# Performance work log

Hardware: AMD Instinct MI355X
Metric: run time of the kernel (lower is better)

The kernel has to match this reference:

```python
import jax, jax.numpy as jnp
import numpy as np

B, S, D = 2, 2048, 2048
H, DK, DV, L = 16, 128, 128, 64


def setup_inputs() -> dict:
    key = jax.random.key(0)
    ks = jax.random.split(key, 12)
    s = lambda k, shape, fan_in: jax.random.normal(k, shape, jnp.float32) / np.sqrt(fan_in)
    return {
        "queries": jax.random.normal(ks[0], (B, S, D), jnp.float32),
        "keys": jax.random.normal(ks[1], (B, S, D), jnp.float32),
        "values": jax.random.normal(ks[2], (B, S, D), jnp.float32),
        "Wq": s(ks[3], (D, H * DK), D), "bq": jnp.zeros((H * DK,), jnp.float32),
        "Wlk": s(ks[4], (D, H * L), D), "blk": jnp.zeros((H * L,), jnp.float32),
        "Wlv": s(ks[5], (D, H * L), D), "blv": jnp.zeros((H * L,), jnp.float32),
        "Wkr": s(ks[6], (L, DK), L),
        "Wvr": s(ks[7], (L, DV), L),
        "Wout": s(ks[8], (H * DV, D), H * DV), "bout": jnp.zeros((D,), jnp.float32),
    }


def reference(queries, keys, values, Wq, bq, Wlk, blk, Wlv, blv, Wkr, Wvr, Wout, bout):
    b, sq, _ = queries.shape
    sk = keys.shape[1]
    # projections -> [b, h, s, d]
    q = (queries @ Wq + bq).reshape(b, sq, H, DK).transpose(0, 2, 1, 3)
    lk = (keys @ Wlk + blk).reshape(b, sk, H, L).transpose(0, 2, 1, 3)
    lv = (values @ Wlv + blv).reshape(b, sk, H, L).transpose(0, 2, 1, 3)
    k = lk @ Wkr  # [b,h,sk,DK] latent -> key reconstruction
    v = lv @ Wvr  # [b,h,sk,DV]
    scores = jnp.einsum('bhqd,bhkd->bhqk', q, k) / np.sqrt(DK).astype(np.float32)
    causal = jnp.triu(jnp.ones((sq, sk), dtype=bool), k=1)
    scores = jnp.where(causal, -jnp.inf, scores)
    attn = jax.nn.softmax(scores, axis=-1)
    out = jnp.einsum('bhqk,bhkd->bhqd', attn, v)
    out = out.transpose(0, 2, 1, 3).reshape(b, sq, H * DV)
    return out @ Wout + bout
```

## Files before the change

### kernel.cpp

```cpp
#include <hip/hip_runtime.h>
#include <cstdint>
#include <cstddef>

typedef _Float16 f16;
typedef __attribute__((ext_vector_type(8))) _Float16 f16x8;
typedef __attribute__((ext_vector_type(4))) _Float16 f16x4;
typedef __attribute__((ext_vector_type(4))) float f32x4;

constexpr int kB  = 2;
constexpr int kS  = 2048;
constexpr int kD  = 2048;
constexpr int kH  = 16;
constexpr int kL  = 64;
constexpr int kHL = kH * kL;
constexpr int kBS = kB * kS;

__device__ __forceinline__ void load_lds16(const void* g, void* l) {
  __builtin_amdgcn_global_load_lds((const __attribute__((address_space(1))) void*)g,
                                   (__attribute__((address_space(3))) void*)l, 16, 0, 0);
}

__device__ __forceinline__ f32x4 mfma16(f16x8 a, f16x8 b, f32x4 c) {
  return __builtin_amdgcn_mfma_f32_16x16x32_f16(a, b, c, 0, 0, 0);
}

__global__ void cast4(const float* __restrict__ a, const float* __restrict__ b,
                      const float* __restrict__ c, const float* __restrict__ d,
                      f16* __restrict__ oa, f16* __restrict__ ob,
                      f16* __restrict__ oc, f16* __restrict__ od) {
  const int z = blockIdx.z;
  int i = blockIdx.x * 256 + threadIdx.x;
  if (z == 3 && i >= kD * kD / 4) return;
  const float* in = z == 0 ? a : z == 1 ? b : z == 2 ? c : d;
  f16* out = z == 0 ? oa : z == 1 ? ob : z == 2 ? oc : od;
  float4 f = ((const float4*)in)[i];
  f16x4 o; o[0] = (f16)f.x; o[1] = (f16)f.y; o[2] = (f16)f.z; o[3] = (f16)f.w;
  ((f16x4*)out)[i] = o;
}

__device__ __forceinline__ void transpose_body(const float* __restrict__ in,
                                               f16* __restrict__ out, int R, int C) {
  const int r0 = blockIdx.y * 64, c0 = blockIdx.x * 64;
  __shared__ float tile[64][65];
  const int t = threadIdx.x;
  const int cc = t & 63, rr = t >> 6;
#pragma unroll
  for (int p = 0; p < 16; p++) {
    int r = p * 4 + rr;
    tile[r][cc] = in[(size_t)(r0 + r) * C + c0 + cc];
  }
  __syncthreads();
#pragma unroll
  for (int p = 0; p < 16; p++) {
    int c = p * 4 + rr;
    out[(size_t)(c0 + c) * R + r0 + cc] = (f16)tile[cc][c];
  }
}

__global__ __launch_bounds__(256) void transpose3(const float* __restrict__ Wlk,
                                                  const float* __restrict__ Wlv,
                                                  const float* __restrict__ Wout,
                                                  f16* __restrict__ Wlkt,
                                                  f16* __restrict__ Wlvt,
                                                  f16* __restrict__ WoutT) {
  const int z = blockIdx.z;
  if (z < 2 && blockIdx.x >= 16) return;
  if (z == 0) transpose_body(Wlk, Wlkt, 2048, 1024);
  else if (z == 1) transpose_body(Wlv, Wlvt, 2048, 1024);
  else transpose_body(Wout, WoutT, 2048, 2048);
}

__global__ void fold_bq(const float* __restrict__ bq, const float* __restrict__ Wkr,
                        float* __restrict__ bql) {
  int hl = blockIdx.x * 256 + threadIdx.x;
  if (hl >= kHL) return;
  int h = hl >> 6, l = hl & 63;
  float s = 0.f;
  for (int c = 0; c < 128; c++) s += bq[h * 128 + c] * Wkr[l * 128 + c];
  bql[hl] = s;
}

__global__ __launch_bounds__(256) void fold2(const float* __restrict__ Wkr,
                                             const float* __restrict__ Wvr,
                                             const f16* __restrict__ Wq16,
                                             const f16* __restrict__ WoutT,
                                             f16* __restrict__ Wqlt,
                                             f16* __restrict__ W2t) {
  __shared__ f16 sA[64 * 136];
  __shared__ f16 sB[128 * 128];
  const int z = blockIdx.z;
  const int h = blockIdx.y;
  const int d0 = blockIdx.x * 128;
  const float* Wsm = z ? Wvr : Wkr;
  const f16* Bsrc = (z ? WoutT : Wq16) + h * 128;
  const int tid = threadIdx.x;
  const int w = tid >> 6, lane = tid & 63;
  const int quad = lane >> 4, l16 = lane & 15;

#pragma unroll
  for (int it = 0; it < 8; it++) {
    int i = it * 256 + tid;
    float4 f = ((const float4*)Wsm)[i];
    int e = i * 4, r = e >> 7, c = e & 127;
    f16x4 o; o[0] = (f16)f.x; o[1] = (f16)f.y; o[2] = (f16)f.z; o[3] = (f16)f.w;
    *(f16x4*)&sA[r * 136 + c] = o;
  }
#pragma unroll
  for (int c = 0; c < 8; c++) {
    int rbase = w * 32 + c * 4;
    load_lds16(Bsrc + (size_t)(d0 + rbase + (lane >> 4)) * 2048 + (lane & 15) * 8,
               &sB[rbase * 128]);
  }
  __syncthreads();

  if (z == 0) {
    f32x4 acc[4][2];
    for (int mt = 0; mt < 4; mt++)
      for (int nt = 0; nt < 2; nt++) acc[mt][nt] = (f32x4){0.f, 0.f, 0.f, 0.f};
#pragma unroll
    for (int ks = 0; ks < 4; ks++) {
      f16x8 af[4], bf[2];
#pragma unroll
      for (int mt = 0; mt < 4; mt++)
        af[mt] = *(const f16x8*)&sA[(mt * 16 + l16) * 136 + ks * 32 + quad * 8];
#pragma unroll
      for (int nt = 0; nt < 2; nt++)
        bf[nt] = *(const f16x8*)&sB[(w * 32 + nt * 16 + l16) * 128 + ks * 32 + quad * 8];
#pragma unroll
      for (int mt = 0; mt < 4; mt++)
#pragma unroll
        for (int nt = 0; nt < 2; nt++) acc[mt][nt] = mfma16(af[mt], bf[nt], acc[mt][nt]);
    }
#pragma unroll
    for (int mt = 0; mt < 4; mt++)
#pragma unroll
      for (int nt = 0; nt < 2; nt++)
#pragma unroll
        for (int r = 0; r < 4; r++) {
          int row = mt * 16 + quad * 4 + r;
          int col = d0 + w * 32 + nt * 16 + l16;
          Wqlt[(size_t)(h * 64 + row) * 2048 + col] = (f16)acc[mt][nt][r];
        }
  } else {
    f32x4 acc[2][4];
    for (int mt = 0; mt < 2; mt++)
      for (int nt = 0; nt < 4; nt++) acc[mt][nt] = (f32x4){0.f, 0.f, 0.f, 0.f};
#pragma unroll
    for (int ks = 0; ks < 4; ks++) {
      f16x8 af[2], bf[4];
#pragma unroll
      for (int mt = 0; mt < 2; mt++)
        af[mt] = *(const f16x8*)&sB[(w * 32 + mt * 16 + l16) * 128 + ks * 32 + quad * 8];
#pragma unroll
      for (int nt = 0; nt < 4; nt++)
        bf[nt] = *(const f16x8*)&sA[(nt * 16 + l16) * 136 + ks * 32 + quad * 8];
#pragma unroll
      for (int mt = 0; mt < 2; mt++)
#pragma unroll
        for (int nt = 0; nt < 4; nt++) acc[mt][nt] = mfma16(af[mt], bf[nt], acc[mt][nt]);
    }
#pragma unroll
    for (int mt = 0; mt < 2; mt++)
#pragma unroll
      for (int nt = 0; nt < 4; nt++)
#pragma unroll
        for (int r = 0; r < 4; r++) {
          int row = d0 + w * 32 + mt * 16 + quad * 4 + r;
          int col = nt * 16 + l16;
          W2t[(size_t)row * 1024 + h * 64 + col] = (f16)acc[mt][nt][r];
        }
  }
}

template <typename OutT, bool HAS_BIAS>
__device__ __forceinline__ void gemm8p_body(const f16* __restrict__ A, const f16* __restrict__ Bt,
                                            const float* __restrict__ bias, OutT* __restrict__ C,
                                            int N, int K, int m0, int n0) {
  __shared__ f16 sA[3 * 256 * 64];
  __shared__ f16 sB[3 * 128 * 64];
  const int tid = threadIdx.x;
  const int w = tid >> 6, lane = tid & 63;
  const int quad = lane >> 4, l16 = lane & 15;
  const int wm = w >> 2, wn = w & 3;
  const int sw0 = ((quad ^ (l16 & 7)) << 3);
  const int sw1 = (((4 + quad) ^ (l16 & 7)) << 3);

  const int srow = lane >> 3;
  const int schunk = (lane & 7) ^ srow;
  const f16* aG = A + (size_t)(m0 + w * 8 + srow) * K + schunk * 8;
  const f16* bG = Bt + (size_t)(n0 + w * 8 + srow) * K + schunk * 8;
  const int ldsOff = (w * 8) * 64 + lane * 8;

  f32x4 acc[8][2];
#pragma unroll
  for (int i = 0; i < 8; i++) {
    acc[i][0] = (f32x4){0.f, 0.f, 0.f, 0.f};
    acc[i][1] = (f32x4){0.f, 0.f, 0.f, 0.f};
  }

#define STAGE_A(b, k0, j) load_lds16(aG + (size_t)((j) * 64) * K + (k0), \
                                     &sA[(b) * 16384 + (j) * 4096 + ldsOff])
#define STAGE_B(b, k0, j) load_lds16(bG + (size_t)((j) * 64) * K + (k0), \
                                     &sB[(b) * 8192 + (j) * 4096 + ldsOff])
#define PHASE_PRE()  do { __builtin_amdgcn_sched_barrier(0); __builtin_amdgcn_s_barrier(); \
    asm volatile("s_waitcnt lgkmcnt(0)" ::: "memory"); __builtin_amdgcn_sched_barrier(0); \
    __builtin_amdgcn_s_setprio(1); } while (0)
#define PHASE_POST() do { __builtin_amdgcn_s_setprio(0); __builtin_amdgcn_sched_barrier(0); \
    __builtin_amdgcn_s_barrier(); } while (0)

  const int nt = K >> 6;
#pragma unroll
  for (int j = 0; j < 4; j++) STAGE_A(0, 0, j);
  STAGE_B(0, 0, 0); STAGE_B(0, 0, 1);
#pragma unroll
  for (int j = 0; j < 4; j++) STAGE_A(1, 64, j);
  STAGE_B(1, 64, 0); STAGE_B(1, 64, 1);
  asm volatile("s_waitcnt vmcnt(6)" ::: "memory");
  __builtin_amdgcn_sched_barrier(0);
  __builtin_amdgcn_s_barrier();
  __builtin_amdgcn_sched_barrier(0);

  int bc = 0, bs = 2;
  for (int t = 0; t < nt; ++t) {
    const f16* a = &sA[bc * 16384];
    const f16* b = &sB[bc * 8192];
    const bool st = (t + 2) < nt;
    const int kS = (t + 2) << 6;
    f16x8 af[8], bf;

#pragma unroll
    for (int mt = 0; mt < 8; mt++)
      af[mt] = *(const f16x8*)&a[(wm * 128 + mt * 16 + l16) * 64 + sw0];
    bf = *(const f16x8*)&b[(wn * 32 + l16) * 64 + sw0];
    if (st) { STAGE_A(bs, kS, 0); STAGE_A(bs, kS, 1); }
    PHASE_PRE();
#pragma unroll
    for (int mt = 0; mt < 8; mt++) acc[mt][0] = mfma16(af[mt], bf, acc[mt][0]);
    PHASE_POST();

    bf = *(const f16x8*)&b[(wn * 32 + 16 + l16) * 64 + sw0];
    if (st) { STAGE_A(bs, kS, 2); STAGE_A(bs, kS, 3); }
    PHASE_PRE();
#pragma unroll
    for (int mt = 0; mt < 8; mt++) acc[mt][1] = mfma16(af[mt], bf, acc[mt][1]);
    PHASE_POST();

#pragma unroll
    for (int mt = 0; mt < 8; mt++)
      af[mt] = *(const f16x8*)&a[(wm * 128 + mt * 16 + l16) * 64 + sw1];
    bf = *(const f16x8*)&b[(wn * 32 + l16) * 64 + sw1];
    if (st) STAGE_B(bs, kS, 0);
    PHASE_PRE();
#pragma unroll
    for (int mt = 0; mt < 8; mt++) acc[mt][0] = mfma16(af[mt], bf, acc[mt][0]);
    PHASE_POST();

    bf = *(const f16x8*)&b[(wn * 32 + 16 + l16) * 64 + sw1];
    if (st) STAGE_B(bs, kS, 1);
    PHASE_PRE();
#pragma unroll
    for (int mt = 0; mt < 8; mt++) acc[mt][1] = mfma16(af[mt], bf, acc[mt][1]);
    __builtin_amdgcn_s_setprio(0);
    if (t + 1 < nt) {
      if (st) asm volatile("s_waitcnt vmcnt(6)" ::: "memory");
      else    asm volatile("s_waitcnt vmcnt(0)" ::: "memory");
    }
    __builtin_amdgcn_sched_barrier(0);
    __builtin_amdgcn_s_barrier();
    __builtin_amdgcn_sched_barrier(0);

    bc = bc == 2 ? 0 : bc + 1;
    bs = bs == 2 ? 0 : bs + 1;
  }
#undef STAGE_A
#undef STAGE_B
#undef PHASE_PRE
#undef PHASE_POST

#pragma unroll
  for (int mt = 0; mt < 8; mt++) {
#pragma unroll
    for (int nh = 0; nh < 2; nh++) {
      int col = n0 + wn * 32 + nh * 16 + l16;
      float bv = HAS_BIAS ? bias[col] : 0.f;
#pragma unroll
      for (int r = 0; r < 4; r++) {
        int row = m0 + wm * 128 + mt * 16 + quad * 4 + r;
        C[(size_t)row * N + col] = (OutT)(acc[mt][nh][r] + bv);
      }
    }
  }
}

__device__ __forceinline__ int xcd_swizzle(int flat, int nwg) {
  const int cpx = nwg >> 3;
  return (flat & 7) * cpx + (flat >> 3);
}

__global__ __launch_bounds__(512) void gemm3_f16(
    const f16* __restrict__ A0, const f16* __restrict__ A1, const f16* __restrict__ A2,
    const f16* __restrict__ B0, const f16* __restrict__ B1, const f16* __restrict__ B2,
    const float* __restrict__ c0, const float* __restrict__ c1, const float* __restrict__ c2,
    f16* __restrict__ C0, f16* __restrict__ C1, f16* __restrict__ C2, int N, int K) {
  const f16* A = blockIdx.z == 0 ? A0 : blockIdx.z == 1 ? A1 : A2;
  const f16* Bt = blockIdx.z == 0 ? B0 : blockIdx.z == 1 ? B1 : B2;
  const float* bias = blockIdx.z == 0 ? c0 : blockIdx.z == 1 ? c1 : c2;
  f16* C = blockIdx.z == 0 ? C0 : blockIdx.z == 1 ? C1 : C2;
  const int nx = gridDim.x;
  int swz = xcd_swizzle(blockIdx.y * nx + blockIdx.x, nx * gridDim.y);
  gemm8p_body<f16, true>(A, Bt, bias, C, N, K, (swz / nx) * 256, (swz % nx) * 128);
}

__global__ __launch_bounds__(512) void gemm_f32(const f16* __restrict__ A,
                                                const f16* __restrict__ Bt,
                                                const float* __restrict__ bias,
                                                float* __restrict__ C, int N, int K) {
  const int nx = gridDim.x;
  int swz = xcd_swizzle(blockIdx.y * nx + blockIdx.x, nx * gridDim.y);
  gemm8p_body<float, true>(A, Bt, bias, C, N, K, (swz / nx) * 256, (swz % nx) * 128);
}

__global__ __launch_bounds__(256) void transpose_lv(const f16* __restrict__ LV,
                                                    f16* __restrict__ LVt) {
  const int bh = blockIdx.y, b = bh >> 4, h = bh & 15;
  const int s0 = blockIdx.x * 64;
  __shared__ f16 tile[64][65];
  const int t = threadIdx.x;
  const int c0 = t & 63, r0 = t >> 6;
#pragma unroll
  for (int r = 0; r < 16; r++) {
    int s = r * 4 + r0;
    tile[s][c0] = LV[(size_t)(b * kS + s0 + s) * kHL + h * kL + c0];
  }
  __syncthreads();
#pragma unroll
  for (int r = 0; r < 16; r++) {
    int vl = r * 4 + r0;
    LVt[((size_t)bh * kL + vl) * kS + s0 + c0] = tile[c0][vl];
  }
}

__global__ __launch_bounds__(256) void attn(const f16* __restrict__ Qlat,
                                            const f16* __restrict__ LK,
                                            const f16* __restrict__ LVt,
                                            f16* __restrict__ Ctx) {
  const int bh = blockIdx.y, b = bh >> 4, h = bh & 15;
  const int pair = blockIdx.x;
  const int tid = threadIdx.x;
  const int w = tid >> 6, lane = tid & 63;
  const int quad = lane >> 4, l16 = lane & 15;

  __shared__ f16 sK[2][64 * 64];
  __shared__ f16 sV[2][64 * 64];
  __shared__ f16 sP[4][16 * 72];

  const f16* qbase = Qlat + (size_t)b * kS * kHL + h * kL;
  const f16* kbase = LK + (size_t)b * kS * kHL + h * kL;
  const f16* vbase = LVt + (size_t)bh * kL * kS;

  const float cscale = 0.08838834764831845f * 1.4426950408889634f;
  const int rowA = lane >> 3;
  const int colSw = (((lane & 7) ^ (lane >> 3)) << 3);
  const int sw0 = ((quad ^ (l16 & 7)) << 3);
  const int sw1 = (((4 + quad) ^ (l16 & 7)) << 3);

  for (int which = 0; which < 2; which++) {
    const int t = which ? (31 - pair) : pair;
    const int q0 = t * 64;
    const int qrow = q0 + w * 16 + l16;
    const int qg = qrow;
    const int ntile = t + 1;

    f16x8 aq[2];
#pragma unroll
    for (int ks = 0; ks < 2; ks++)
      aq[ks] = *(const f16x8*)(qbase + (size_t)qrow * kHL + ks * 32 + quad * 8);

    f32x4 acc[4];
    for (int nt = 0; nt < 4; nt++) acc[nt] = (f32x4){0.f, 0.f, 0.f, 0.f};
    float m_s = -3.0e38f;
    float l_part = 0.f;

    __syncthreads();
    {
      const int rl = w * 16;
      load_lds16(kbase + (size_t)(rl + rowA) * kHL + colSw, &sK[0][rl * 64]);
      load_lds16(vbase + (size_t)(rl + rowA) * kS + colSw, &sV[0][rl * 64]);
      load_lds16(kbase + (size_t)(rl + 8 + rowA) * kHL + colSw, &sK[0][(rl + 8) * 64]);
      load_lds16(vbase + (size_t)(rl + 8 + rowA) * kS + colSw, &sV[0][(rl + 8) * 64]);
    }
    int cur = 0;

    for (int it = 0; it < ntile; ++it) {
      const int kv0 = it * 64;
      __syncthreads();

      if (it + 1 < ntile) {
        const int nkv = kv0 + 64;
        f16* dK = &sK[cur ^ 1][0];
        f16* dV = &sV[cur ^ 1][0];
        const int rl = w * 16;
        load_lds16(kbase + (size_t)(nkv + rl + rowA) * kHL + colSw, dK + rl * 64);
        load_lds16(vbase + (size_t)(rl + rowA) * kS + nkv + colSw, dV + rl * 64);
        load_lds16(kbase + (size_t)(nkv + rl + 8 + rowA) * kHL + colSw, dK + (rl + 8) * 64);
        load_lds16(vbase + (size_t)(rl + 8 + rowA) * kS + nkv + colSw, dV + (rl + 8) * 64);
      }
      const f16* sKc = &sK[cur][0];
      const f16* sVc = &sV[cur][0];

      f32x4 sc[4];
      for (int nt = 0; nt < 4; nt++) sc[nt] = (f32x4){0.f, 0.f, 0.f, 0.f};
#pragma unroll
      for (int ks = 0; ks < 2; ks++) {
        const int sw = ks ? sw1 : sw0;
        f16x8 bk[4];
#pragma unroll
        for (int nt = 0; nt < 4; nt++)
          bk[nt] = *(const f16x8*)&sKc[(nt * 16 + l16) * 64 + sw];
        __builtin_amdgcn_s_setprio(1);
#pragma unroll
        for (int nt = 0; nt < 4; nt++) sc[nt] = mfma16(bk[nt], aq[ks], sc[nt]);
        __builtin_amdgcn_s_setprio(0);
      }

      if (kv0 == q0) {
#pragma unroll
        for (int nt = 0; nt < 4; nt++) {
#pragma unroll
          for (int r = 0; r < 4; r++) {
            int kvg = kv0 + nt * 16 + quad * 4 + r;
            if (kvg > qg) sc[nt][r] = -1.0e30f;
          }
        }
      }

      float tm = -3.0e38f;
#pragma unroll
      for (int nt = 0; nt < 4; nt++)
        tm = fmaxf(tm, fmaxf(fmaxf(sc[nt][0], sc[nt][1]), fmaxf(sc[nt][2], sc[nt][3])));
      tm = fmaxf(tm, __shfl_xor(tm, 16));
      tm = fmaxf(tm, __shfl_xor(tm, 32));
      const float tms = tm * cscale;

      if (!__all(tms <= m_s)) {
        const float mnew = fmaxf(m_s, tms);
        const float alpha = __builtin_amdgcn_exp2f(m_s - mnew);
        m_s = mnew;
        l_part *= alpha;
        float ar[4];
#pragma unroll
        for (int r = 0; r < 4; r++) ar[r] = __shfl(alpha, quad * 4 + r);
#pragma unroll
        for (int nt = 0; nt < 4; nt++)
#pragma unroll
          for (int r = 0; r < 4; r++) acc[nt][r] *= ar[r];
      }

      float ps = 0.f;
#pragma unroll
      for (int nt = 0; nt < 4; nt++) {
        f16x4 pk;
#pragma unroll
        for (int r = 0; r < 4; r++) {
          float p = __builtin_amdgcn_exp2f(__builtin_fmaf(sc[nt][r], cscale, -m_s));
          ps += p;
          pk[r] = (f16)p;
        }
        *(f16x4*)&sP[w][l16 * 72 + nt * 16 + quad * 4] = pk;
      }
      l_part += ps;

#pragma unroll
      for (int ks = 0; ks < 2; ks++) {
        const int sw = ks ? sw1 : sw0;
        f16x8 ap = *(const f16x8*)&sP[w][l16 * 72 + ks * 32 + quad * 8];
        f16x8 bv[4];
#pragma unroll
        for (int nt = 0; nt < 4; nt++)
          bv[nt] = *(const f16x8*)&sVc[(nt * 16 + l16) * 64 + sw];
        __builtin_amdgcn_s_setprio(1);
#pragma unroll
        for (int nt = 0; nt < 4; nt++) acc[nt] = mfma16(ap, bv[nt], acc[nt]);
        __builtin_amdgcn_s_setprio(0);
      }
      cur ^= 1;
    }

    float lfull = l_part;
    lfull += __shfl_xor(lfull, 16);
    lfull += __shfl_xor(lfull, 32);
    float inv[4];
#pragma unroll
    for (int r = 0; r < 4; r++) inv[r] = 1.f / __shfl(lfull, quad * 4 + r);
#pragma unroll
    for (int r = 0; r < 4; r++) {
      int qout = q0 + w * 16 + quad * 4 + r;
      size_t base = (size_t)(b * kS + qout) * kHL + h * kL;
#pragma unroll
      for (int nt = 0; nt < 4; nt++)
        Ctx[base + nt * 16 + l16] = (f16)(acc[nt][r] * inv[r]);
    }
  }
}

extern "C" void kernel_launch(void* const* d_in, const int* in_sizes, int n_in,
                              void* d_out, int out_size, void* d_ws, size_t ws_size,
                              hipStream_t stream) {
  (void)in_sizes; (void)n_in; (void)out_size; (void)ws_size;
  const float* queries = (const float*)d_in[0];
  const float* keys    = (const float*)d_in[1];
  const float* values  = (const float*)d_in[2];
  const float* Wq      = (const float*)d_in[3];
  const float* bq      = (const float*)d_in[4];
  const float* Wlk     = (const float*)d_in[5];
  const float* blk     = (const float*)d_in[6];
  const float* Wlv     = (const float*)d_in[7];
  const float* blv     = (const float*)d_in[8];
  const float* Wkr     = (const float*)d_in[9];
  const float* Wvr     = (const float*)d_in[10];
  const float* Wout    = (const float*)d_in[11];
  const float* bout    = (const float*)d_in[12];

  char* ws = (char*)d_ws;
  size_t off = 0;
  auto alloc = [&](size_t bytes) {
    void* p = ws + off;
    off += (bytes + 255) & ~(size_t)255;
    return p;
  };
  f16* qb    = (f16*)alloc((size_t)kBS * kD * 2);
  f16* kb    = (f16*)alloc((size_t)kBS * kD * 2);
  f16* vb    = (f16*)alloc((size_t)kBS * kD * 2);
  f16* Wqlt  = (f16*)alloc((size_t)kHL * kD * 2);
  f16* Wlkt  = (f16*)alloc((size_t)kHL * kD * 2);
  f16* Wlvt  = (f16*)alloc((size_t)kHL * kD * 2);
  f16* W2t   = (f16*)alloc((size_t)kD * kHL * 2);
  float* bql = (float*)alloc(kHL * 4);
  f16* Qlat  = (f16*)alloc((size_t)kBS * kHL * 2);
  f16* LKb   = (f16*)alloc((size_t)kBS * kHL * 2);
  f16* LVb   = (f16*)alloc((size_t)kBS * kHL * 2);
  f16* Wq16  = Qlat;
  f16* WoutT = LKb;
  f16* LVtb = qb;
  f16* Ctx  = kb;

  const int n4 = kBS * kD / 4;
  cast4<<<dim3(n4 / 256, 1, 4), 256, 0, stream>>>(queries, keys, values, Wq, qb, kb, vb, Wq16);
  transpose3<<<dim3(32, 32, 3), 256, 0, stream>>>(Wlk, Wlv, Wout, Wlkt, Wlvt, WoutT);
  fold_bq<<<kHL / 256, 256, 0, stream>>>(bq, Wkr, bql);
  fold2<<<dim3(16, 16, 2), 256, 0, stream>>>(Wkr, Wvr, Wq16, WoutT, Wqlt, W2t);

  gemm3_f16<<<dim3(kHL / 128, kBS / 256, 3), 512, 0, stream>>>(
      qb, kb, vb, Wqlt, Wlkt, Wlvt, bql, blk, blv, Qlat, LKb, LVb, kHL, kD);

  transpose_lv<<<dim3(kS / 64, kB * kH), 256, 0, stream>>>(LVb, LVtb);
  attn<<<dim3(16, kB * kH), 256, 0, stream>>>(Qlat, LKb, LVtb, Ctx);
  gemm_f32<<<dim3(kD / 128, kBS / 256), 512, 0, stream>>>(Ctx, W2t, bout, (float*)d_out, kD, kHL);
}
```

Measured before the change: 395.6 us.

## Switch GEMM warp layout to 4x2 with 64x64 per-wave tiles and two phases

Changes the 8-wave arrangement in the 256x128 block GEMM from 2x4 (128x32 per wave) to 4x2 (64x64 per wave), so each wave loads 4 A and 4 B fragments and runs 16 MFMAs per k-half. Each k-step now has two barrier-separated phases instead of four, with global-to-LDS staging regrouped to match. The aim is fewer LDS fragment reads per MFMA and fewer barriers per k-step. In exchange each phase holds more fragment registers live and the epilogue write pattern changes.

After: 364.3 us. 7.9% less time.

```diff
diff --git a/kernel.cpp b/kernel.cpp
--- a/kernel.cpp
+++ b/kernel.cpp
@@ -181,7 +181,7 @@
   const int tid = threadIdx.x;
   const int w = tid >> 6, lane = tid & 63;
   const int quad = lane >> 4, l16 = lane & 15;
-  const int wm = w >> 2, wn = w & 3;
+  const int wm = w >> 1, wn = w & 1;
   const int sw0 = ((quad ^ (l16 & 7)) << 3);
   const int sw1 = (((4 + quad) ^ (l16 & 7)) << 3);
 
@@ -191,30 +191,30 @@
   const f16* bG = Bt + (size_t)(n0 + w * 8 + srow) * K + schunk * 8;
   const int ldsOff = (w * 8) * 64 + lane * 8;
 
-  f32x4 acc[8][2];
-#pragma unroll
-  for (int i = 0; i < 8; i++) {
-    acc[i][0] = (f32x4){0.f, 0.f, 0.f, 0.f};
-    acc[i][1] = (f32x4){0.f, 0.f, 0.f, 0.f};
-  }
-
-#define STAGE_A(b, k0, j) load_lds16(aG + (size_t)((j) * 64) * K + (k0), \
-                                     &sA[(b) * 16384 + (j) * 4096 + ldsOff])
-#define STAGE_B(b, k0, j) load_lds16(bG + (size_t)((j) * 64) * K + (k0), \
-                                     &sB[(b) * 8192 + (j) * 4096 + ldsOff])
-#define PHASE_PRE()  do { __builtin_amdgcn_sched_barrier(0); __builtin_amdgcn_s_barrier(); \
-    asm volatile("s_waitcnt lgkmcnt(0)" ::: "memory"); __builtin_amdgcn_sched_barrier(0); \
-    __builtin_amdgcn_s_setprio(1); } while (0)
-#define PHASE_POST() do { __builtin_amdgcn_s_setprio(0); __builtin_amdgcn_sched_barrier(0); \
-    __builtin_amdgcn_s_barrier(); } while (0)
+  f32x4 acc[4][4];
+#pragma unroll
+  for (int i = 0; i < 4; i++)
+#pragma unroll
+    for (int j = 0; j < 4; j++) acc[i][j] = (f32x4){0.f, 0.f, 0.f, 0.f};
+
+#define STAGE_A4(b, k0) do {                                                   \
+    load_lds16(aG + (k0),                  &sA[(b) * 16384 + ldsOff]);          \
+    load_lds16(aG + (size_t)64 * K + (k0), &sA[(b) * 16384 + 4096 + ldsOff]);   \
+    load_lds16(aG + (size_t)128 * K + (k0), &sA[(b) * 16384 + 8192 + ldsOff]);  \
+    load_lds16(aG + (size_t)192 * K + (k0), &sA[(b) * 16384 + 12288 + ldsOff]); \
+  } while (0)
+#define STAGE_B2(b, k0) do {                                                   \
+    load_lds16(bG + (k0),                  &sB[(b) * 8192 + ldsOff]);           \
+    load_lds16(bG + (size_t)64 * K + (k0), &sB[(b) * 8192 + 4096 + ldsOff]);    \
+  } while (0)
+#define PHASE_SYNC() do { __builtin_amdgcn_sched_barrier(0);                   \
+    __builtin_amdgcn_s_barrier();                                              \
+    asm volatile("s_waitcnt lgkmcnt(0)" ::: "memory");                         \
+    __builtin_amdgcn_sched_barrier(0); } while (0)
 
   const int nt = K >> 6;
-#pragma unroll
-  for (int j = 0; j < 4; j++) STAGE_A(0, 0, j);
-  STAGE_B(0, 0, 0); STAGE_B(0, 0, 1);
-#pragma unroll
-  for (int j = 0; j < 4; j++) STAGE_A(1, 64, j);
-  STAGE_B(1, 64, 0); STAGE_B(1, 64, 1);
+  STAGE_A4(0, 0); STAGE_B2(0, 0);
+  STAGE_A4(1, 64); STAGE_B2(1, 64);
   asm volatile("s_waitcnt vmcnt(6)" ::: "memory");
   __builtin_amdgcn_sched_barrier(0);
   __builtin_amdgcn_s_barrier();
@@ -225,41 +225,39 @@
     const f16* a = &sA[bc * 16384];
     const f16* b = &sB[bc * 8192];
     const bool st = (t + 2) < nt;
-    const int kS = (t + 2) << 6;
-    f16x8 af[8], bf;
-
-#pragma unroll
-    for (int mt = 0; mt < 8; mt++)
-      af[mt] = *(const f16x8*)&a[(wm * 128 + mt * 16 + l16) * 64 + sw0];
-    bf = *(const f16x8*)&b[(wn * 32 + l16) * 64 + sw0];
-    if (st) { STAGE_A(bs, kS, 0); STAGE_A(bs, kS, 1); }
-    PHASE_PRE();
-#pragma unroll
-    for (int mt = 0; mt < 8; mt++) acc[mt][0] = mfma16(af[mt], bf, acc[mt][0]);
-    PHASE_POST();
-
-    bf = *(const f16x8*)&b[(wn * 32 + 16 + l16) * 64 + sw0];
-    if (st) { STAGE_A(bs, kS, 2); STAGE_A(bs, kS, 3); }
-    PHASE_PRE();
-#pragma unroll
-    for (int mt = 0; mt < 8; mt++) acc[mt][1] = mfma16(af[mt], bf, acc[mt][1]);
-    PHASE_POST();
-
-#pragma unroll
-    for (int mt = 0; mt < 8; mt++)
-      af[mt] = *(const f16x8*)&a[(wm * 128 + mt * 16 + l16) * 64 + sw1];
-    bf = *(const f16x8*)&b[(wn * 32 + l16) * 64 + sw1];
-    if (st) STAGE_B(bs, kS, 0);
-    PHASE_PRE();
-#pragma unroll
-    for (int mt = 0; mt < 8; mt++) acc[mt][0] = mfma16(af[mt], bf, acc[mt][0]);
-    PHASE_POST();
-
-    bf = *(const f16x8*)&b[(wn * 32 + 16 + l16) * 64 + sw1];
-    if (st) STAGE_B(bs, kS, 1);
-    PHASE_PRE();
-#pragma unroll
-    for (int mt = 0; mt < 8; mt++) acc[mt][1] = mfma16(af[mt], bf, acc[mt][1]);
+    const int kN = (t + 2) << 6;
+    f16x8 af[4], bf[4];
+
+#pragma unroll
+    for (int mt = 0; mt < 4; mt++)
+      af[mt] = *(const f16x8*)&a[(wm * 64 + mt * 16 + l16) * 64 + sw0];
+#pragma unroll
+    for (int nf = 0; nf < 4; nf++)
+      bf[nf] = *(const f16x8*)&b[(wn * 64 + nf * 16 + l16) * 64 + sw0];
+    if (st) STAGE_A4(bs, kN);
+    PHASE_SYNC();
+    __builtin_amdgcn_s_setprio(1);
+#pragma unroll
+    for (int mt = 0; mt < 4; mt++)
+#pragma unroll
+      for (int nf = 0; nf < 4; nf++) acc[mt][nf] = mfma16(af[mt], bf[nf], acc[mt][nf]);
+    __builtin_amdgcn_s_setprio(0);
+    __builtin_amdgcn_sched_barrier(0);
+    __builtin_amdgcn_s_barrier();
+
+#pragma unroll
+    for (int mt = 0; mt < 4; mt++)
+      af[mt] = *(const f16x8*)&a[(wm * 64 + mt * 16 + l16) * 64 + sw1];
+#pragma unroll
+    for (int nf = 0; nf < 4; nf++)
+      bf[nf] = *(const f16x8*)&b[(wn * 64 + nf * 16 + l16) * 64 + sw1];
+    if (st) STAGE_B2(bs, kN);
+    PHASE_SYNC();
+    __builtin_amdgcn_s_setprio(1);
+#pragma unroll
+    for (int mt = 0; mt < 4; mt++)
+#pragma unroll
+      for (int nf = 0; nf < 4; nf++) acc[mt][nf] = mfma16(af[mt], bf[nf], acc[mt][nf]);
     __builtin_amdgcn_s_setprio(0);
     if (t + 1 < nt) {
       if (st) asm volatile("s_waitcnt vmcnt(6)" ::: "memory");
@@ -272,21 +270,20 @@
     bc = bc == 2 ? 0 : bc + 1;
     bs = bs == 2 ? 0 : bs + 1;
   }
-#undef STAGE_A
-#undef STAGE_B
-#undef PHASE_PRE
-#undef PHASE_POST
-
-#pragma unroll
-  for (int mt = 0; mt < 8; mt++) {
-#pragma unroll
-    for (int nh = 0; nh < 2; nh++) {
-      int col = n0 + wn * 32 + nh * 16 + l16;
+#undef STAGE_A4
+#undef STAGE_B2
+#undef PHASE_SYNC
+
+#pragma unroll
+  for (int mt = 0; mt < 4; mt++) {
+#pragma unroll
+    for (int nf = 0; nf < 4; nf++) {
+      int col = n0 + wn * 64 + nf * 16 + l16;
       float bv = HAS_BIAS ? bias[col] : 0.f;
 #pragma unroll
       for (int r = 0; r < 4; r++) {
-        int row = m0 + wm * 128 + mt * 16 + quad * 4 + r;
-        C[(size_t)row * N + col] = (OutT)(acc[mt][nh][r] + bv);
+        int row = m0 + wm * 64 + mt * 16 + quad * 4 + r;
+        C[(size_t)row * N + col] = (OutT)(acc[mt][nf][r] + bv);
       }
     }
   }
```
